# Kernel tuning notes

Hardware: AMD Instinct MI355X
Metric: run time of the kernel (lower is better)

Reference implementation:

```python
import jax, jax.numpy as jnp
import numpy as np

BN_EPS = 1e-5  # torch BatchNorm1d default


def setup_inputs() -> dict:
    key = jax.random.key(0)
    ks = jax.random.split(key, 4)
    B, C, N, O = 8, 64, 4096, 64
    x = jax.random.normal(ks[0], (B, C, N, 1), dtype=jnp.float32)
    w1 = jax.random.normal(ks[1], (C, O), dtype=jnp.float32) * (1.0 / np.sqrt(C))
    b1 = jnp.zeros((O,), jnp.float32)
    gamma = jnp.ones((O,), jnp.float32)
    beta = jnp.zeros((O,), jnp.float32)
    w2 = jax.random.normal(ks[2], (O, O), dtype=jnp.float32) * (1.0 / np.sqrt(O))
    b2 = jnp.zeros((O,), jnp.float32)
    eps_gin = jnp.zeros((), jnp.float32)  # train_eps=True, init eps=0.0
    return {"x": x, "w1": w1, "b1": b1, "gamma": gamma, "beta": beta,
            "w2": w2, "b2": b2, "eps_gin": eps_gin, "k": 16}


def _knn_idx(xf, k):
    # xf: [B, N, C] -> indices of k nearest neighbors (incl. self, loop=True)
    sq = jnp.sum(xf * xf, axis=-1)                       # [B, N]
    d = sq[:, :, None] + sq[:, None, :] - 2.0 * jnp.einsum('bnc,bmc->bnm', xf, xf)
    _, idx = jax.lax.top_k(-d, k)                        # [B, N, k]
    return idx


def reference(x, w1, b1, gamma, beta, w2, b2, eps_gin, k):
    B, C, N, _ = x.shape
    xf = jnp.transpose(x[..., 0], (0, 2, 1))             # [B, N, C]
    idx = _knn_idx(xf, k)                                # [B, N, k]
    # GIN aggregation: each node has exactly k neighbors -> gather + sum
    gathered = jax.vmap(lambda xb, ib: xb[ib])(xf, idx)  # [B, N, k, C]
    aggr = gathered.sum(axis=2)                          # [B, N, C]
    h = (1.0 + eps_gin) * xf + aggr                      # [B, N, C]
    hf = h.reshape(B * N, C)
    h1 = hf @ w1 + b1                                    # [B*N, O]
    # BatchNorm1d, training-mode batch statistics (biased variance)
    mean = jnp.mean(h1, axis=0)
    var = jnp.mean((h1 - mean) ** 2, axis=0)
    hn = gamma * (h1 - mean) / jnp.sqrt(var + BN_EPS) + beta
    hg = jax.nn.gelu(hn, approximate=False)              # torch default GELU (erf)
    out = hg @ w2 + b2                                   # [B*N, O]
    return jnp.transpose(out.reshape(B, N, -1), (0, 2, 1))[..., None]  # [B, O, N, 1]
```

## Files before the change

### kernel.cpp

```cpp
#include <hip/hip_runtime.h>
#include <cstdint>
#include <cstddef>

#define B_ 8
#define C_ 64
#define N_ 4096
#define O_ 64
#define ROWS_ (B_*N_)
#define NSPLIT_ 2
#define CAPB_ 33

typedef unsigned long long u64;
typedef unsigned int u32;
typedef unsigned short u16;
typedef __attribute__((ext_vector_type(8))) short bf16x8;
typedef __attribute__((ext_vector_type(16))) float f32x16;

#define MFMA32(A,Bv,Cv) __builtin_amdgcn_mfma_f32_32x32x16_bf16(A,Bv,Cv,0,0,0)

#define OFF_XF   0
#define OFF_SQ   8388608
#define OFF_KD   8519680
#define OFF_KI   16908288
#define OFF_PACK 21102592
#define OFF_IDX  33685504
#define OFF_H    8519680
#define OFF_H1   16908288
#define OFF_BN   25296896

__device__ __forceinline__ void insert16(u64 kv[16], u64 key) {
  if (key < kv[15]) {
#pragma unroll
    for (int j = 15; j > 0; --j) {
      u64 a = kv[j-1], b = kv[j];
      kv[j] = (key < a) ? a : ((key < b) ? key : b);
    }
    kv[0] = (key < kv[0]) ? key : kv[0];
  }
}

__global__ __launch_bounds__(256) void k_transpose(const float* __restrict__ x,
                                                   float* __restrict__ xf,
                                                   float* __restrict__ sq,
                                                   u16* __restrict__ pack) {
  __shared__ float lds[64 * 65];
  const int b  = blockIdx.x >> 6;
  const int n0 = (blockIdx.x & 63) << 6;
  const int tid = threadIdx.x;
  const float* xb = x + (size_t)b * C_ * N_;
  {
    const int nn = tid & 63;
    const int c0 = tid >> 6;
#pragma unroll
    for (int i = 0; i < 16; ++i) {
      int c = c0 + i * 4;
      lds[c * 65 + nn] = xb[(size_t)c * N_ + n0 + nn];
    }
  }
  __syncthreads();
  {
    const int cc  = tid & 63;
    const int nn0 = tid >> 6;
#pragma unroll
    for (int i = 0; i < 16; ++i) {
      int nn = nn0 + i * 4;
      xf[((size_t)(b * N_ + n0 + nn)) * 64 + cc] = lds[cc * 65 + nn];
    }
  }
  if (tid < 64) {
    float s = 0.f;
#pragma unroll
    for (int c = 0; c < 64; ++c) { float v = lds[c * 65 + tid]; s += v * v; }
    sq[b * N_ + n0 + tid] = s;
  }
  {
    const int lane = tid & 63;
    const int slice = tid >> 6;
    const int kb = slice * 16 + (lane >> 5) * 8;
#pragma unroll
    for (int tl = 0; tl < 2; ++tl) {
      const int nl = tl * 32 + (lane & 31);
      bf16x8 H, M, L;
#pragma unroll
      for (int j = 0; j < 8; ++j) {
        float f = lds[(kb + j) * 65 + nl];
        u32 u = __float_as_uint(f);
        u32 rh = (u + 0x7FFFu + ((u >> 16) & 1u)) >> 16;
        float bh = __uint_as_float(rh << 16);
        float f1 = f - bh;
        u = __float_as_uint(f1);
        u32 rm = (u + 0x7FFFu + ((u >> 16) & 1u)) >> 16;
        float bm = __uint_as_float(rm << 16);
        float f2 = f1 - bm;
        u = __float_as_uint(f2);
        u32 rl = (u + 0x7FFFu + ((u >> 16) & 1u)) >> 16;
        H[j] = (short)rh; M[j] = (short)rm; L[j] = (short)rl;
      }
      const int tile = ((blockIdx.x & 63) << 1) + tl;
      u16* basep = pack + ((size_t)(b * 128 + tile) * 12) * 512 + lane * 8;
      *(bf16x8*)(basep + (size_t)(0 + slice) * 512) = H;
      *(bf16x8*)(basep + (size_t)(4 + slice) * 512) = M;
      *(bf16x8*)(basep + (size_t)(8 + slice) * 512) = L;
    }
  }
}

#define KNN_LOAD(P, mt) do { const u16* ap_ = pb + (size_t)(mt) * (12*512); \
  P##h0 = *(const bf16x8*)(ap_ + 0*512);  P##h1 = *(const bf16x8*)(ap_ + 1*512); \
  P##h2 = *(const bf16x8*)(ap_ + 2*512);  P##h3 = *(const bf16x8*)(ap_ + 3*512); \
  P##m0 = *(const bf16x8*)(ap_ + 4*512);  P##m1 = *(const bf16x8*)(ap_ + 5*512); \
  P##m2 = *(const bf16x8*)(ap_ + 6*512);  P##m3 = *(const bf16x8*)(ap_ + 7*512); \
  P##l0 = *(const bf16x8*)(ap_ + 8*512);  P##l1 = *(const bf16x8*)(ap_ + 9*512); \
  P##l2 = *(const bf16x8*)(ap_ +10*512);  P##l3 = *(const bf16x8*)(ap_ +11*512); } while(0)

#define SQ_LOAD(MT) do { const float* sp_ = sqb + (MT) * 32 + 4 * h; \
  sv0 = *(const float4*)(sp_);      sv1 = *(const float4*)(sp_ + 8); \
  sv2 = *(const float4*)(sp_ + 16); sv3 = *(const float4*)(sp_ + 24); } while(0)

#define KNN_MFMA(P) \
  acc0 = MFMA32(P##h0, ql0, acc0);  acc1 = MFMA32(P##h1, ql1, acc1); \
  acc0 = MFMA32(P##l0, qh0, acc0);  acc1 = MFMA32(P##l1, qh1, acc1); \
  acc0 = MFMA32(P##m0, qm0, acc0);  acc1 = MFMA32(P##m1, qm1, acc1); \
  acc0 = MFMA32(P##h0, qm0, acc0);  acc1 = MFMA32(P##h1, qm1, acc1); \
  acc0 = MFMA32(P##m0, qh0, acc0);  acc1 = MFMA32(P##m1, qh1, acc1); \
  acc0 = MFMA32(P##h0, qh0, acc0);  acc1 = MFMA32(P##h1, qh1, acc1); \
  acc0 = MFMA32(P##h2, ql2, acc0);  acc1 = MFMA32(P##h3, ql3, acc1); \
  acc0 = MFMA32(P##l2, qh2, acc0);  acc1 = MFMA32(P##l3, qh3, acc1); \
  acc0 = MFMA32(P##m2, qm2, acc0);  acc1 = MFMA32(P##m3, qm3, acc1); \
  acc0 = MFMA32(P##h2, qm2, acc0);  acc1 = MFMA32(P##h3, qm3, acc1); \
  acc0 = MFMA32(P##m2, qh2, acc0);  acc1 = MFMA32(P##m3, qh3, acc1); \
  acc0 = MFMA32(P##h2, qh2, acc0);  acc1 = MFMA32(P##h3, qh3, acc1);

#define SEL_T8() do { \
  float sqv_[16] = {sv0.x, sv0.y, sv0.z, sv0.w, sv1.x, sv1.y, sv1.z, sv1.w, \
                    sv2.x, sv2.y, sv2.z, sv2.w, sv3.x, sv3.y, sv3.z, sv3.w}; \
_Pragma("unroll") \
  for (int r_ = 0; r_ < 16; ++r_) { \
    float d_ = fmaf(-2.f, acc0[r_] + acc1[r_], sqv_[r_]); \
    u32 u_ = __float_as_uint(d_); \
    u_ ^= ((int)u_ < 0) ? 0xFFFFFFFFu : 0x80000000u; \
    if (u_ < kv1[7]) { \
_Pragma("unroll") \
      for (int j_ = 7; j_ > 0; --j_) { \
        u32 a_ = kv1[j_-1], b_ = kv1[j_]; \
        kv1[j_] = (u_ < a_) ? a_ : ((u_ < b_) ? u_ : b_); \
      } \
      kv1[0] = (u_ < kv1[0]) ? u_ : kv1[0]; \
    } \
  } \
} while(0)

#define SEL_C(MT) do { \
  const u32 ic_ = (u32)((MT) * 32 + 4 * h); \
  float sqv_[16] = {sv0.x, sv0.y, sv0.z, sv0.w, sv1.x, sv1.y, sv1.z, sv1.w, \
                    sv2.x, sv2.y, sv2.z, sv2.w, sv3.x, sv3.y, sv3.z, sv3.w}; \
_Pragma("unroll") \
  for (int r_ = 0; r_ < 16; ++r_) { \
    float d_ = fmaf(-2.f, acc0[r_] + acc1[r_], sqv_[r_]); \
    u32 u_ = __float_as_uint(d_); \
    u_ ^= ((int)u_ < 0) ? 0xFFFFFFFFu : 0x80000000u; \
    if (u_ <= tauk) { \
      myc[cnt] = ((u64)u_ << 32) | (u64)(ic_ + (u32)((r_ & 3) + 8 * (r_ >> 2))); \
      ++cnt; \
    } \
  } \
  if (__any(cnt >= CAPB_ - 16)) {             \
    for (int i_ = 0; i_ < cnt; ++i_) insert16(kv, myc[i_]); \
    cnt = 0; \
  } \
} while(0)

__global__ __launch_bounds__(256, 2) void k_knn(const u16* __restrict__ pack,
                                                const float* __restrict__ sq,
                                                u32* __restrict__ kd,
                                                u16* __restrict__ ki) {
  __shared__ u64 cand[256 * CAPB_];
  const int bx = blockIdx.x;
  const int split = bx & 1;
  const int qb = (bx >> 1) & 31;
  const int b = bx >> 6;
  const int tid = threadIdx.x;
  const int lane = tid & 63;
  const int wid = tid >> 6;
  const int qt = qb * 4 + wid;
  const int h = lane >> 5;
  const u16* pb = pack + (size_t)b * (128 * 12 * 512) + lane * 8;

  const u16* qp = pb + (size_t)qt * (12 * 512);
  bf16x8 qh0 = *(const bf16x8*)(qp + 0*512), qh1 = *(const bf16x8*)(qp + 1*512);
  bf16x8 qh2 = *(const bf16x8*)(qp + 2*512), qh3 = *(const bf16x8*)(qp + 3*512);
  bf16x8 qm0 = *(const bf16x8*)(qp + 4*512), qm1 = *(const bf16x8*)(qp + 5*512);
  bf16x8 qm2 = *(const bf16x8*)(qp + 6*512), qm3 = *(const bf16x8*)(qp + 7*512);
  bf16x8 ql0 = *(const bf16x8*)(qp + 8*512), ql1 = *(const bf16x8*)(qp + 9*512);
  bf16x8 ql2 = *(const bf16x8*)(qp + 10*512), ql3 = *(const bf16x8*)(qp + 11*512);

  const float* sqb = sq + b * N_;
  const int mbase = split * 64;

  bf16x8 Ah0, Ah1, Ah2, Ah3, Am0, Am1, Am2, Am3, Al0, Al1, Al2, Al3;
  bf16x8 Bh0, Bh1, Bh2, Bh3, Bm0, Bm1, Bm2, Bm3, Bl0, Bl1, Bl2, Bl3;
  float4 sv0, sv1, sv2, sv3;

  u32 kv1[8];
#pragma unroll
  for (int j = 0; j < 8; ++j) kv1[j] = 0xFF800000u;

  KNN_LOAD(A, mbase);
  for (int ct = 0; ct < 8; ct += 2) {
    SQ_LOAD(mbase + ct);
    KNN_LOAD(B, mbase + ct + 1);
    {
      f32x16 acc0 = {0,0,0,0,0,0,0,0,0,0,0,0,0,0,0,0};
      f32x16 acc1 = {0,0,0,0,0,0,0,0,0,0,0,0,0,0,0,0};
      KNN_MFMA(A)
      SEL_T8();
    }
    SQ_LOAD(mbase + ct + 1);
    KNN_LOAD(A, mbase + ct + 2);
    {
      f32x16 acc0 = {0,0,0,0,0,0,0,0,0,0,0,0,0,0,0,0};
      f32x16 acc1 = {0,0,0,0,0,0,0,0,0,0,0,0,0,0,0,0};
      KNN_MFMA(B)
      SEL_T8();
    }
  }
  u32 tk = kv1[7];
  u32 pk = (u32)__shfl_xor((int)tk, 32);
  const u32 tauk = (tk > pk) ? tk : pk;

  u64 kv[16];
#pragma unroll
  for (int j = 0; j < 16; ++j) kv[j] = 0xFF8000000000FFFFull;
  int cnt = 0;
  u64* myc = cand + tid * CAPB_;

  KNN_LOAD(A, mbase);
  for (int ct = 0; ct < 64; ct += 2) {
    SQ_LOAD(mbase + ct);
    KNN_LOAD(B, mbase + ct + 1);
    {
      f32x16 acc0 = {0,0,0,0,0,0,0,0,0,0,0,0,0,0,0,0};
      f32x16 acc1 = {0,0,0,0,0,0,0,0,0,0,0,0,0,0,0,0};
      KNN_MFMA(A)
      SEL_C(mbase + ct);
    }
    SQ_LOAD(mbase + ct + 1);
    KNN_LOAD(A, mbase + ((ct + 2) & 63));
    {
      f32x16 acc0 = {0,0,0,0,0,0,0,0,0,0,0,0,0,0,0,0};
      f32x16 acc1 = {0,0,0,0,0,0,0,0,0,0,0,0,0,0,0,0};
      KNN_MFMA(B)
      SEL_C(mbase + ct + 1);
    }
  }
  for (int i = 0; i < cnt; ++i) insert16(kv, myc[i]);

  u64 m[16];
#pragma unroll
  for (int j = 0; j < 16; ++j) {
    u64 p = __shfl_xor(kv[15 - j], 32);
    m[j] = (kv[j] < p) ? kv[j] : p;
  }
#pragma unroll
  for (int d = 8; d >= 1; d >>= 1) {
#pragma unroll
    for (int j = 0; j < 16; ++j) {
      if ((j & d) == 0) {
        u64 a = m[j], c = m[j | d];
        m[j] = (a < c) ? a : c;
        m[j | d] = (a < c) ? c : a;
      }
    }
  }

  if (lane < 32) {
    const int row = b * N_ + qt * 32 + lane;
    u32* dp = kd + ((size_t)row * NSPLIT_ + split) * 16;
    u16* ip = ki + ((size_t)row * NSPLIT_ + split) * 16;
#pragma unroll
    for (int j = 0; j < 16; ++j) {
      dp[j] = (u32)(m[j] >> 32);
      ip[j] = (u16)(m[j] & 0xFFFFu);
    }
  }
}

__global__ __launch_bounds__(256) void k_merge(const u32* __restrict__ kd,
                                               const u16* __restrict__ ki,
                                               int* __restrict__ knn,
                                               float* __restrict__ bn_acc) {
  int tid = threadIdx.x;
  if (blockIdx.x == 0 && tid < 128) bn_acc[tid] = 0.f;
  int r = blockIdx.x * 256 + tid;
  const u32* dp = kd + (size_t)r * (NSPLIT_ * 16);
  const u16* ip = ki + (size_t)r * (NSPLIT_ * 16);
  u64 a[16], b[16];
#pragma unroll
  for (int j = 0; j < 16; ++j) {
    a[j] = ((u64)dp[j] << 32) | ip[j];
    b[j] = ((u64)dp[16 + j] << 32) | ip[16 + j];
  }
#pragma unroll
  for (int j = 0; j < 16; ++j) {
    u64 x = a[j], y = b[15 - j];
    knn[r * 16 + j] = (int)((x < y ? x : y) & 0xFFFFu);
  }
}

__global__ __launch_bounds__(256) void k_aggr(const float* __restrict__ xf,
                                              const int* __restrict__ knn,
                                              const float* __restrict__ eps_gin,
                                              float* __restrict__ h) {
  const int tid = threadIdx.x;
  const int r = blockIdx.x * 4 + (tid >> 6);
  const int c = tid & 63;
  const int b = r >> 12;
  const float* xfb = xf + (size_t)b * N_ * 64;
  const float eps = eps_gin[0];
  float v = (1.f + eps) * xf[(size_t)r * 64 + c];
  const int* kn = knn + r * 16;
#pragma unroll
  for (int j = 0; j < 16; ++j) {
    int m = kn[j];
    v += xfb[(size_t)m * 64 + c];
  }
  h[(size_t)r * 64 + c] = v;
}

__global__ __launch_bounds__(256) void k_gemm1(const float* __restrict__ h,
                                               const float* __restrict__ w1,
                                               const float* __restrict__ b1,
                                               float* __restrict__ h1,
                                               float* __restrict__ bn_acc) {
  __shared__ float w[64 * 64];
  __shared__ float rs[4][64], rs2[4][64];
  const int tid = threadIdx.x;
#pragma unroll
  for (int i = 0; i < 16; ++i) w[tid + i * 256] = w1[tid + i * 256];
  __syncthreads();
  const int o = tid & 63;
  const int q = tid >> 6;
  const int r0 = blockIdx.x * 64;
  const float bias = b1[o];
  float s = 0.f, s2 = 0.f;
#pragma unroll
  for (int i = 0; i < 16; ++i) {
    int row = r0 + q + i * 4;
    const float* hr = h + (size_t)row * 64;
    float acc = bias;
#pragma unroll
    for (int c = 0; c < 64; ++c) acc += hr[c] * w[c * 64 + o];
    h1[(size_t)row * 64 + o] = acc;
    s += acc; s2 += acc * acc;
  }
  rs[q][o] = s; rs2[q][o] = s2;
  __syncthreads();
  if (tid < 64) {
    float ts  = rs[0][tid] + rs[1][tid] + rs[2][tid] + rs[3][tid];
    float ts2 = rs2[0][tid] + rs2[1][tid] + rs2[2][tid] + rs2[3][tid];
    atomicAdd(&bn_acc[tid], ts);
    atomicAdd(&bn_acc[64 + tid], ts2);
  }
}

__global__ void k_bnfin(const float* __restrict__ bn_acc,
                        const float* __restrict__ gamma,
                        const float* __restrict__ beta,
                        float* __restrict__ bn_par) {
  int o = threadIdx.x;
  const float inv = 1.f / (float)ROWS_;
  float mean = bn_acc[o] * inv;
  float var  = bn_acc[64 + o] * inv - mean * mean;
  float sc = gamma[o] * rsqrtf(var + 1e-5f);
  bn_par[o] = sc;
  bn_par[64 + o] = beta[o] - mean * sc;
}

__global__ __launch_bounds__(256) void k_final(const float* __restrict__ h1,
                                               const float* __restrict__ bn_par,
                                               const float* __restrict__ w2,
                                               const float* __restrict__ b2,
                                               float* __restrict__ out) {
  __shared__ float w[64 * 64];
  __shared__ float hg[64 * 65];
  const int tid = threadIdx.x;
#pragma unroll
  for (int i = 0; i < 16; ++i) w[tid + i * 256] = w2[tid + i * 256];
  const int r0 = blockIdx.x * 64;
  const int b  = r0 >> 12;
  const int n0 = r0 & (N_ - 1);
  const int o = tid & 63;
  const int q = tid >> 6;
  const float sc = bn_par[o], sh = bn_par[64 + o];
#pragma unroll
  for (int i = 0; i < 16; ++i) {
    int rl = q + i * 4;
    float v = h1[(size_t)(r0 + rl) * 64 + o] * sc + sh;
    float g = 0.5f * v * (1.f + erff(v * 0.70710678118654752f));
    hg[rl * 65 + o] = g;
  }
  __syncthreads();
  const int nl = tid & 63;
#pragma unroll
  for (int i = 0; i < 16; ++i) {
    int o2 = q + i * 4;
    float acc = b2[o2];
#pragma unroll
    for (int oo = 0; oo < 64; ++oo) acc += hg[nl * 65 + oo] * w[oo * 64 + o2];
    out[((size_t)(b * 64 + o2)) * N_ + n0 + nl] = acc;
  }
}

extern "C" void kernel_launch(void* const* d_in, const int* in_sizes, int n_in,
                              void* d_out, int out_size, void* d_ws, size_t ws_size,
                              hipStream_t stream) {
  const float* x     = (const float*)d_in[0];
  const float* w1    = (const float*)d_in[1];
  const float* b1    = (const float*)d_in[2];
  const float* gamma = (const float*)d_in[3];
  const float* beta  = (const float*)d_in[4];
  const float* w2    = (const float*)d_in[5];
  const float* b2    = (const float*)d_in[6];
  const float* eps_g = (const float*)d_in[7];
  float* out = (float*)d_out;

  char* ws = (char*)d_ws;
  float* xf   = (float*)(ws + OFF_XF);
  float* sq   = (float*)(ws + OFF_SQ);
  u32*   kd   = (u32*)  (ws + OFF_KD);
  u16*   ki   = (u16*)  (ws + OFF_KI);
  u16*   pack = (u16*)  (ws + OFF_PACK);
  int*   knn  = (int*)  (ws + OFF_IDX);
  float* h    = (float*)(ws + OFF_H);
  float* h1   = (float*)(ws + OFF_H1);
  float* bn_acc = (float*)(ws + OFF_BN);
  float* bn_par = (float*)(ws + OFF_BN + 512);

  k_transpose<<<512, 256, 0, stream>>>(x, xf, sq, pack);
  k_knn<<<512, 256, 0, stream>>>(pack, sq, kd, ki);
  k_merge<<<ROWS_ / 256, 256, 0, stream>>>(kd, ki, knn, bn_acc);
  k_aggr<<<ROWS_ / 4, 256, 0, stream>>>(xf, knn, eps_g, h);
  k_gemm1<<<ROWS_ / 64, 256, 0, stream>>>(h, w1, b1, h1, bn_acc);
  k_bnfin<<<1, 64, 0, stream>>>(bn_acc, gamma, beta, bn_par);
  k_final<<<ROWS_ / 64, 256, 0, stream>>>(h1, bn_par, w2, b2, out);
}
```

Before: 367.4 us.

## Split kNN search four ways with a slimmer register pipeline and four-way merge

Each batch's candidate range is now split into four parts instead of two, and the kNN grid doubles to 1024 blocks. The two accumulators are replaced by one, and operands are loaded per k-slice into two small register sets, so the kernel can ask for three blocks per CU instead of two. The candidate buffer in shared memory is split into separate u32 distance and u16 index arrays, and the threshold test is done on the raw float before the key conversion. The merge kernel now combines four sorted partial lists with bitonic steps, which adds merge work and more partial-result traffic.

```diff
diff --git a/kernel.cpp b/kernel.cpp
--- a/kernel.cpp
+++ b/kernel.cpp
@@ -7,8 +7,10 @@
 #define N_ 4096
 #define O_ 64
 #define ROWS_ (B_*N_)
-#define NSPLIT_ 2
-#define CAPB_ 33
+#define NSPLIT_ 4
+#define CAPB_ 25
+#define DRAIN_AT_ 9
+#define TAU_TILES_ 12
 
 typedef unsigned long long u64;
 typedef unsigned int u32;
@@ -105,38 +107,40 @@
   }
 }
 
-#define KNN_LOAD(P, mt) do { const u16* ap_ = pb + (size_t)(mt) * (12*512); \
-  P##h0 = *(const bf16x8*)(ap_ + 0*512);  P##h1 = *(const bf16x8*)(ap_ + 1*512); \
-  P##h2 = *(const bf16x8*)(ap_ + 2*512);  P##h3 = *(const bf16x8*)(ap_ + 3*512); \
-  P##m0 = *(const bf16x8*)(ap_ + 4*512);  P##m1 = *(const bf16x8*)(ap_ + 5*512); \
-  P##m2 = *(const bf16x8*)(ap_ + 6*512);  P##m3 = *(const bf16x8*)(ap_ + 7*512); \
-  P##l0 = *(const bf16x8*)(ap_ + 8*512);  P##l1 = *(const bf16x8*)(ap_ + 9*512); \
-  P##l2 = *(const bf16x8*)(ap_ +10*512);  P##l3 = *(const bf16x8*)(ap_ +11*512); } while(0)
+#define LOADS(P, mt, s) do { const u16* ap_ = pb + (size_t)(mt) * (12*512) + (size_t)(s) * 512; \
+  P##h = *(const bf16x8*)(ap_);          \
+  P##m = *(const bf16x8*)(ap_ + 4*512);  \
+  P##l = *(const bf16x8*)(ap_ + 8*512);  } while(0)
+
+#define MFMAS(P, S) \
+  acc = MFMA32(P##h, ql##S, acc); \
+  acc = MFMA32(P##l, qh##S, acc); \
+  acc = MFMA32(P##m, qm##S, acc); \
+  acc = MFMA32(P##h, qm##S, acc); \
+  acc = MFMA32(P##m, qh##S, acc); \
+  acc = MFMA32(P##h, qh##S, acc);
 
 #define SQ_LOAD(MT) do { const float* sp_ = sqb + (MT) * 32 + 4 * h; \
   sv0 = *(const float4*)(sp_);      sv1 = *(const float4*)(sp_ + 8); \
   sv2 = *(const float4*)(sp_ + 16); sv3 = *(const float4*)(sp_ + 24); } while(0)
 
-#define KNN_MFMA(P) \
-  acc0 = MFMA32(P##h0, ql0, acc0);  acc1 = MFMA32(P##h1, ql1, acc1); \
-  acc0 = MFMA32(P##l0, qh0, acc0);  acc1 = MFMA32(P##l1, qh1, acc1); \
-  acc0 = MFMA32(P##m0, qm0, acc0);  acc1 = MFMA32(P##m1, qm1, acc1); \
-  acc0 = MFMA32(P##h0, qm0, acc0);  acc1 = MFMA32(P##h1, qm1, acc1); \
-  acc0 = MFMA32(P##m0, qh0, acc0);  acc1 = MFMA32(P##m1, qh1, acc1); \
-  acc0 = MFMA32(P##h0, qh0, acc0);  acc1 = MFMA32(P##h1, qh1, acc1); \
-  acc0 = MFMA32(P##h2, ql2, acc0);  acc1 = MFMA32(P##h3, ql3, acc1); \
-  acc0 = MFMA32(P##l2, qh2, acc0);  acc1 = MFMA32(P##l3, qh3, acc1); \
-  acc0 = MFMA32(P##m2, qm2, acc0);  acc1 = MFMA32(P##m3, qm3, acc1); \
-  acc0 = MFMA32(P##h2, qm2, acc0);  acc1 = MFMA32(P##h3, qm3, acc1); \
-  acc0 = MFMA32(P##m2, qh2, acc0);  acc1 = MFMA32(P##m3, qh3, acc1); \
-  acc0 = MFMA32(P##h2, qh2, acc0);  acc1 = MFMA32(P##h3, qh3, acc1);
+#define TILE_MFMA(MT, NXT) \
+  LOADS(P1, (MT), 1); \
+  MFMAS(P0, 0) \
+  LOADS(P0, (MT), 2); \
+  MFMAS(P1, 1) \
+  LOADS(P1, (MT), 3); \
+  MFMAS(P0, 2) \
+  SQ_LOAD(MT); \
+  LOADS(P0, (NXT), 0); \
+  MFMAS(P1, 3)
 
 #define SEL_T8() do { \
   float sqv_[16] = {sv0.x, sv0.y, sv0.z, sv0.w, sv1.x, sv1.y, sv1.z, sv1.w, \
                     sv2.x, sv2.y, sv2.z, sv2.w, sv3.x, sv3.y, sv3.z, sv3.w}; \
 _Pragma("unroll") \
   for (int r_ = 0; r_ < 16; ++r_) { \
-    float d_ = fmaf(-2.f, acc0[r_] + acc1[r_], sqv_[r_]); \
+    float d_ = fmaf(-2.f, acc[r_], sqv_[r_]); \
     u32 u_ = __float_as_uint(d_); \
     u_ ^= ((int)u_ < 0) ? 0xFFFFFFFFu : 0x80000000u; \
     if (u_ < kv1[7]) { \
@@ -150,35 +154,42 @@
   } \
 } while(0)
 
+#define DRAINC() do { \
+  for (int i_ = 0; i_ < cnt; ++i_) { \
+    u64 key_ = ((u64)myK[i_] << 32) | (u64)myI[i_]; \
+    insert16(kv, key_); \
+  } \
+  cnt = 0; \
+} while(0)
+
 #define SEL_C(MT) do { \
   const u32 ic_ = (u32)((MT) * 32 + 4 * h); \
   float sqv_[16] = {sv0.x, sv0.y, sv0.z, sv0.w, sv1.x, sv1.y, sv1.z, sv1.w, \
                     sv2.x, sv2.y, sv2.z, sv2.w, sv3.x, sv3.y, sv3.z, sv3.w}; \
 _Pragma("unroll") \
   for (int r_ = 0; r_ < 16; ++r_) { \
-    float d_ = fmaf(-2.f, acc0[r_] + acc1[r_], sqv_[r_]); \
-    u32 u_ = __float_as_uint(d_); \
-    u_ ^= ((int)u_ < 0) ? 0xFFFFFFFFu : 0x80000000u; \
-    if (u_ <= tauk) { \
-      myc[cnt] = ((u64)u_ << 32) | (u64)(ic_ + (u32)((r_ & 3) + 8 * (r_ >> 2))); \
+    float d_ = fmaf(-2.f, acc[r_], sqv_[r_]); \
+    if (d_ <= tauF) {                        \
+      u32 u_ = __float_as_uint(d_); \
+      u_ ^= ((int)u_ < 0) ? 0xFFFFFFFFu : 0x80000000u; \
+      myK[cnt] = u_; \
+      myI[cnt] = (u16)(ic_ + (u32)((r_ & 3) + 8 * (r_ >> 2))); \
       ++cnt; \
     } \
   } \
-  if (__any(cnt >= CAPB_ - 16)) {             \
-    for (int i_ = 0; i_ < cnt; ++i_) insert16(kv, myc[i_]); \
-    cnt = 0; \
-  } \
+  if (__any(cnt >= DRAIN_AT_)) DRAINC(); \
 } while(0)
 
-__global__ __launch_bounds__(256, 2) void k_knn(const u16* __restrict__ pack,
+__global__ __launch_bounds__(256, 3) void k_knn(const u16* __restrict__ pack,
                                                 const float* __restrict__ sq,
                                                 u32* __restrict__ kd,
                                                 u16* __restrict__ ki) {
-  __shared__ u64 cand[256 * CAPB_];
+  __shared__ u32 candK[256 * CAPB_];
+  __shared__ u16 candI[256 * CAPB_];
   const int bx = blockIdx.x;
-  const int split = bx & 1;
-  const int qb = (bx >> 1) & 31;
-  const int b = bx >> 6;
+  const int qb = bx & 31;
+  const int split = (bx >> 5) & 3;
+  const int b = bx >> 7;
   const int tid = threadIdx.x;
   const int lane = tid & 63;
   const int wid = tid >> 6;
@@ -195,92 +206,70 @@
   bf16x8 ql2 = *(const bf16x8*)(qp + 10*512), ql3 = *(const bf16x8*)(qp + 11*512);
 
   const float* sqb = sq + b * N_;
-  const int mbase = split * 64;
-
-  bf16x8 Ah0, Ah1, Ah2, Ah3, Am0, Am1, Am2, Am3, Al0, Al1, Al2, Al3;
-  bf16x8 Bh0, Bh1, Bh2, Bh3, Bm0, Bm1, Bm2, Bm3, Bl0, Bl1, Bl2, Bl3;
+  const int mbase = split * 32;
+
+  bf16x8 P0h, P0m, P0l, P1h, P1m, P1l;
   float4 sv0, sv1, sv2, sv3;
 
   u32 kv1[8];
 #pragma unroll
   for (int j = 0; j < 8; ++j) kv1[j] = 0xFF800000u;
 
-  KNN_LOAD(A, mbase);
-  for (int ct = 0; ct < 8; ct += 2) {
-    SQ_LOAD(mbase + ct);
-    KNN_LOAD(B, mbase + ct + 1);
-    {
-      f32x16 acc0 = {0,0,0,0,0,0,0,0,0,0,0,0,0,0,0,0};
-      f32x16 acc1 = {0,0,0,0,0,0,0,0,0,0,0,0,0,0,0,0};
-      KNN_MFMA(A)
-      SEL_T8();
-    }
-    SQ_LOAD(mbase + ct + 1);
-    KNN_LOAD(A, mbase + ct + 2);
-    {
-      f32x16 acc0 = {0,0,0,0,0,0,0,0,0,0,0,0,0,0,0,0};
-      f32x16 acc1 = {0,0,0,0,0,0,0,0,0,0,0,0,0,0,0,0};
-      KNN_MFMA(B)
-      SEL_T8();
-    }
-  }
-  u32 tk = kv1[7];
-  u32 pk = (u32)__shfl_xor((int)tk, 32);
-  const u32 tauk = (tk > pk) ? tk : pk;
-
-  u64 kv[16];
-#pragma unroll
-  for (int j = 0; j < 16; ++j) kv[j] = 0xFF8000000000FFFFull;
-  int cnt = 0;
-  u64* myc = cand + tid * CAPB_;
-
-  KNN_LOAD(A, mbase);
-  for (int ct = 0; ct < 64; ct += 2) {
-    SQ_LOAD(mbase + ct);
-    KNN_LOAD(B, mbase + ct + 1);
-    {
-      f32x16 acc0 = {0,0,0,0,0,0,0,0,0,0,0,0,0,0,0,0};
-      f32x16 acc1 = {0,0,0,0,0,0,0,0,0,0,0,0,0,0,0,0};
-      KNN_MFMA(A)
+  LOADS(P0, mbase, 0);
+  for (int ct = 0; ct < TAU_TILES_; ++ct) {
+    f32x16 acc = {0,0,0,0,0,0,0,0,0,0,0,0,0,0,0,0};
+    TILE_MFMA(mbase + ct, mbase + ct + 1)
+    SEL_T8();
+  }
+  {
+    u32 tk = kv1[7];
+    u32 pk = (u32)__shfl_xor((int)tk, 32);
+    if (pk > tk) tk = pk;
+    u32 tu = (tk & 0x80000000u) ? (tk ^ 0x80000000u) : ~tk;
+    const float tauF = __uint_as_float(tu);
+
+    u64 kv[16];
+#pragma unroll
+    for (int j = 0; j < 16; ++j) kv[j] = 0xFF8000000000FFFFull;
+    int cnt = 0;
+    u32* myK = candK + tid * CAPB_;
+    u16* myI = candI + tid * CAPB_;
+
+    LOADS(P0, mbase, 0);
+    for (int ct = 0; ct < 32; ++ct) {
+      f32x16 acc = {0,0,0,0,0,0,0,0,0,0,0,0,0,0,0,0};
+      TILE_MFMA(mbase + ct, mbase + ((ct + 1) & 31))
       SEL_C(mbase + ct);
     }
-    SQ_LOAD(mbase + ct + 1);
-    KNN_LOAD(A, mbase + ((ct + 2) & 63));
-    {
-      f32x16 acc0 = {0,0,0,0,0,0,0,0,0,0,0,0,0,0,0,0};
-      f32x16 acc1 = {0,0,0,0,0,0,0,0,0,0,0,0,0,0,0,0};
-      KNN_MFMA(B)
-      SEL_C(mbase + ct + 1);
-    }
-  }
-  for (int i = 0; i < cnt; ++i) insert16(kv, myc[i]);
-
-  u64 m[16];
-#pragma unroll
-  for (int j = 0; j < 16; ++j) {
-    u64 p = __shfl_xor(kv[15 - j], 32);
-    m[j] = (kv[j] < p) ? kv[j] : p;
-  }
-#pragma unroll
-  for (int d = 8; d >= 1; d >>= 1) {
+    DRAINC();
+
+    u64 m[16];
 #pragma unroll
     for (int j = 0; j < 16; ++j) {
-      if ((j & d) == 0) {
-        u64 a = m[j], c = m[j | d];
-        m[j] = (a < c) ? a : c;
-        m[j | d] = (a < c) ? c : a;
+      u64 p = __shfl_xor(kv[15 - j], 32);
+      m[j] = (kv[j] < p) ? kv[j] : p;
+    }
+#pragma unroll
+    for (int d = 8; d >= 1; d >>= 1) {
+#pragma unroll
+      for (int j = 0; j < 16; ++j) {
+        if ((j & d) == 0) {
+          u64 a = m[j], c = m[j | d];
+          m[j] = (a < c) ? a : c;
+          m[j | d] = (a < c) ? c : a;
+        }
       }
     }
-  }
-
-  if (lane < 32) {
-    const int row = b * N_ + qt * 32 + lane;
-    u32* dp = kd + ((size_t)row * NSPLIT_ + split) * 16;
-    u16* ip = ki + ((size_t)row * NSPLIT_ + split) * 16;
-#pragma unroll
-    for (int j = 0; j < 16; ++j) {
-      dp[j] = (u32)(m[j] >> 32);
-      ip[j] = (u16)(m[j] & 0xFFFFu);
+
+    if (lane < 32) {
+      const int row = b * N_ + qt * 32 + lane;
+      u32* dp = kd + ((size_t)row * NSPLIT_ + split) * 16;
+      u16* ip = ki + ((size_t)row * NSPLIT_ + split) * 16;
+#pragma unroll
+      for (int j = 0; j < 16; ++j) {
+        dp[j] = (u32)(m[j] >> 32);
+        ip[j] = (u16)(m[j] & 0xFFFFu);
+      }
     }
   }
 }
@@ -294,15 +283,31 @@
   int r = blockIdx.x * 256 + tid;
   const u32* dp = kd + (size_t)r * (NSPLIT_ * 16);
   const u16* ip = ki + (size_t)r * (NSPLIT_ * 16);
-  u64 a[16], b[16];
+  u64 m1[16], m2[16];
 #pragma unroll
   for (int j = 0; j < 16; ++j) {
-    a[j] = ((u64)dp[j] << 32) | ip[j];
-    b[j] = ((u64)dp[16 + j] << 32) | ip[16 + j];
+    u64 a = ((u64)dp[j] << 32) | ip[j];
+    u64 b = ((u64)dp[16 + (15 - j)] << 32) | ip[16 + (15 - j)];
+    m1[j] = (a < b) ? a : b;
+    u64 c = ((u64)dp[32 + j] << 32) | ip[32 + j];
+    u64 d = ((u64)dp[48 + (15 - j)] << 32) | ip[48 + (15 - j)];
+    m2[j] = (c < d) ? c : d;
+  }
+#pragma unroll
+  for (int dd = 8; dd >= 1; dd >>= 1) {
+#pragma unroll
+    for (int j = 0; j < 16; ++j) {
+      if ((j & dd) == 0) {
+        u64 a = m1[j], c = m1[j | dd];
+        m1[j] = (a < c) ? a : c;  m1[j | dd] = (a < c) ? c : a;
+        u64 e = m2[j], f = m2[j | dd];
+        m2[j] = (e < f) ? e : f;  m2[j | dd] = (e < f) ? f : e;
+      }
+    }
   }
 #pragma unroll
   for (int j = 0; j < 16; ++j) {
-    u64 x = a[j], y = b[15 - j];
+    u64 x = m1[j], y = m2[15 - j];
     knn[r * 16 + j] = (int)((x < y ? x : y) & 0xFFFFu);
   }
 }
@@ -437,7 +442,7 @@
   float* bn_par = (float*)(ws + OFF_BN + 512);
 
   k_transpose<<<512, 256, 0, stream>>>(x, xf, sq, pack);
-  k_knn<<<512, 256, 0, stream>>>(pack, sq, kd, ki);
+  k_knn<<<1024, 256, 0, stream>>>(pack, sq, kd, ki);
   k_merge<<<ROWS_ / 256, 256, 0, stream>>>(kd, ki, knn, bn_acc);
   k_aggr<<<ROWS_ / 4, 256, 0, stream>>>(xf, knn, eps_g, h);
   k_gemm1<<<ROWS_ / 64, 256, 0, stream>>>(h, w1, b1, h1, bn_acc);
```

Result: slower. 417.2 us (+13.6%).

## Software-pipeline KNN MFMA tiles against selection and compare in float domain

Applied to the files above, without the earlier changes.

Restructures the KNN distance loop so the MFMA chain for the next 32-column tile runs while the selection/candidate filtering of the previous tile executes, using two independent accumulators, one per tile, instead of two partial accumulators summed per tile. The candidate filter now compares the raw float distance against a float threshold decoded from the sortable-key tau, so the key transform only runs for accepted candidates. It also simplifies the sign-flip to a branchless shift/or. This aims to hide MFMA latency behind VALU selection work, at the cost of a serial 24-deep MFMA dependency chain per tile, more live registers, and one extra prefetched tile at the loop ends.

```diff
diff --git a/kernel.cpp b/kernel.cpp
--- a/kernel.cpp
+++ b/kernel.cpp
@@ -9,6 +9,7 @@
 #define ROWS_ (B_*N_)
 #define NSPLIT_ 2
 #define CAPB_ 33
+#define TAU_TILES_ 8
 
 typedef unsigned long long u64;
 typedef unsigned int u32;
@@ -105,7 +106,7 @@
   }
 }
 
-#define KNN_LOAD(P, mt) do { const u16* ap_ = pb + (size_t)(mt) * (12*512); \
+#define LOADF(P, mt) do { const u16* ap_ = pb + (size_t)(mt) * (12*512); \
   P##h0 = *(const bf16x8*)(ap_ + 0*512);  P##h1 = *(const bf16x8*)(ap_ + 1*512); \
   P##h2 = *(const bf16x8*)(ap_ + 2*512);  P##h3 = *(const bf16x8*)(ap_ + 3*512); \
   P##m0 = *(const bf16x8*)(ap_ + 4*512);  P##m1 = *(const bf16x8*)(ap_ + 5*512); \
@@ -113,32 +114,32 @@
   P##l0 = *(const bf16x8*)(ap_ + 8*512);  P##l1 = *(const bf16x8*)(ap_ + 9*512); \
   P##l2 = *(const bf16x8*)(ap_ +10*512);  P##l3 = *(const bf16x8*)(ap_ +11*512); } while(0)
 
-#define SQ_LOAD(MT) do { const float* sp_ = sqb + (MT) * 32 + 4 * h; \
-  sv0 = *(const float4*)(sp_);      sv1 = *(const float4*)(sp_ + 8); \
-  sv2 = *(const float4*)(sp_ + 16); sv3 = *(const float4*)(sp_ + 24); } while(0)
-
-#define KNN_MFMA(P) \
-  acc0 = MFMA32(P##h0, ql0, acc0);  acc1 = MFMA32(P##h1, ql1, acc1); \
-  acc0 = MFMA32(P##l0, qh0, acc0);  acc1 = MFMA32(P##l1, qh1, acc1); \
-  acc0 = MFMA32(P##m0, qm0, acc0);  acc1 = MFMA32(P##m1, qm1, acc1); \
-  acc0 = MFMA32(P##h0, qm0, acc0);  acc1 = MFMA32(P##h1, qm1, acc1); \
-  acc0 = MFMA32(P##m0, qh0, acc0);  acc1 = MFMA32(P##m1, qh1, acc1); \
-  acc0 = MFMA32(P##h0, qh0, acc0);  acc1 = MFMA32(P##h1, qh1, acc1); \
-  acc0 = MFMA32(P##h2, ql2, acc0);  acc1 = MFMA32(P##h3, ql3, acc1); \
-  acc0 = MFMA32(P##l2, qh2, acc0);  acc1 = MFMA32(P##l3, qh3, acc1); \
-  acc0 = MFMA32(P##m2, qm2, acc0);  acc1 = MFMA32(P##m3, qm3, acc1); \
-  acc0 = MFMA32(P##h2, qm2, acc0);  acc1 = MFMA32(P##h3, qm3, acc1); \
-  acc0 = MFMA32(P##m2, qh2, acc0);  acc1 = MFMA32(P##m3, qh3, acc1); \
-  acc0 = MFMA32(P##h2, qh2, acc0);  acc1 = MFMA32(P##h3, qh3, acc1);
-
-#define SEL_T8() do { \
-  float sqv_[16] = {sv0.x, sv0.y, sv0.z, sv0.w, sv1.x, sv1.y, sv1.z, sv1.w, \
-                    sv2.x, sv2.y, sv2.z, sv2.w, sv3.x, sv3.y, sv3.z, sv3.w}; \
+#define SQL(V0,V1,V2,V3, MT) do { const float* sp_ = sqb + (MT) * 32 + 4 * h; \
+  V0 = *(const float4*)(sp_);      V1 = *(const float4*)(sp_ + 8); \
+  V2 = *(const float4*)(sp_ + 16); V3 = *(const float4*)(sp_ + 24); } while(0)
+
+#define TILE24(P, ACC) \
+  ACC = MFMA32(P##h0, ql0, kz);   ACC = MFMA32(P##l0, qh0, ACC); \
+  ACC = MFMA32(P##m0, qm0, ACC);  ACC = MFMA32(P##h0, qm0, ACC); \
+  ACC = MFMA32(P##m0, qh0, ACC);  ACC = MFMA32(P##h0, qh0, ACC); \
+  ACC = MFMA32(P##h1, ql1, ACC);  ACC = MFMA32(P##l1, qh1, ACC); \
+  ACC = MFMA32(P##m1, qm1, ACC);  ACC = MFMA32(P##h1, qm1, ACC); \
+  ACC = MFMA32(P##m1, qh1, ACC);  ACC = MFMA32(P##h1, qh1, ACC); \
+  ACC = MFMA32(P##h2, ql2, ACC);  ACC = MFMA32(P##l2, qh2, ACC); \
+  ACC = MFMA32(P##m2, qm2, ACC);  ACC = MFMA32(P##h2, qm2, ACC); \
+  ACC = MFMA32(P##m2, qh2, ACC);  ACC = MFMA32(P##h2, qh2, ACC); \
+  ACC = MFMA32(P##h3, ql3, ACC);  ACC = MFMA32(P##l3, qh3, ACC); \
+  ACC = MFMA32(P##m3, qm3, ACC);  ACC = MFMA32(P##h3, qm3, ACC); \
+  ACC = MFMA32(P##m3, qh3, ACC);  ACC = MFMA32(P##h3, qh3, ACC);
+
+#define SEL_T8(ACC, V0,V1,V2,V3) do { \
+  float sqv_[16] = {V0.x, V0.y, V0.z, V0.w, V1.x, V1.y, V1.z, V1.w, \
+                    V2.x, V2.y, V2.z, V2.w, V3.x, V3.y, V3.z, V3.w}; \
 _Pragma("unroll") \
   for (int r_ = 0; r_ < 16; ++r_) { \
-    float d_ = fmaf(-2.f, acc0[r_] + acc1[r_], sqv_[r_]); \
+    float d_ = fmaf(-2.f, ACC[r_], sqv_[r_]); \
     u32 u_ = __float_as_uint(d_); \
-    u_ ^= ((int)u_ < 0) ? 0xFFFFFFFFu : 0x80000000u; \
+    u_ ^= ((u32)((int)u_ >> 31)) | 0x80000000u; \
     if (u_ < kv1[7]) { \
 _Pragma("unroll") \
       for (int j_ = 7; j_ > 0; --j_) { \
@@ -150,21 +151,21 @@
   } \
 } while(0)
 
-#define SEL_C(MT) do { \
+#define SEL_C(ACC, V0,V1,V2,V3, MT) do { \
   const u32 ic_ = (u32)((MT) * 32 + 4 * h); \
-  float sqv_[16] = {sv0.x, sv0.y, sv0.z, sv0.w, sv1.x, sv1.y, sv1.z, sv1.w, \
-                    sv2.x, sv2.y, sv2.z, sv2.w, sv3.x, sv3.y, sv3.z, sv3.w}; \
+  float sqv_[16] = {V0.x, V0.y, V0.z, V0.w, V1.x, V1.y, V1.z, V1.w, \
+                    V2.x, V2.y, V2.z, V2.w, V3.x, V3.y, V3.z, V3.w}; \
 _Pragma("unroll") \
   for (int r_ = 0; r_ < 16; ++r_) { \
-    float d_ = fmaf(-2.f, acc0[r_] + acc1[r_], sqv_[r_]); \
-    u32 u_ = __float_as_uint(d_); \
-    u_ ^= ((int)u_ < 0) ? 0xFFFFFFFFu : 0x80000000u; \
-    if (u_ <= tauk) { \
+    float d_ = fmaf(-2.f, ACC[r_], sqv_[r_]); \
+    if (d_ <= tauF) { \
+      u32 u_ = __float_as_uint(d_); \
+      u_ ^= ((u32)((int)u_ >> 31)) | 0x80000000u; \
       myc[cnt] = ((u64)u_ << 32) | (u64)(ic_ + (u32)((r_ & 3) + 8 * (r_ >> 2))); \
       ++cnt; \
     } \
   } \
-  if (__any(cnt >= CAPB_ - 16)) {             \
+  if (__any(cnt >= CAPB_ - 16)) {           \
     for (int i_ = 0; i_ < cnt; ++i_) insert16(kv, myc[i_]); \
     cnt = 0; \
   } \
@@ -196,37 +197,35 @@
 
   const float* sqb = sq + b * N_;
   const int mbase = split * 64;
+  const f32x16 kz = {0,0,0,0,0,0,0,0,0,0,0,0,0,0,0,0};
 
   bf16x8 Ah0, Ah1, Ah2, Ah3, Am0, Am1, Am2, Am3, Al0, Al1, Al2, Al3;
   bf16x8 Bh0, Bh1, Bh2, Bh3, Bm0, Bm1, Bm2, Bm3, Bl0, Bl1, Bl2, Bl3;
-  float4 sv0, sv1, sv2, sv3;
+  float4 sa0, sa1, sa2, sa3, sb0, sb1, sb2, sb3;
+  f32x16 acc0, acc1;
 
   u32 kv1[8];
 #pragma unroll
   for (int j = 0; j < 8; ++j) kv1[j] = 0xFF800000u;
 
-  KNN_LOAD(A, mbase);
-  for (int ct = 0; ct < 8; ct += 2) {
-    SQ_LOAD(mbase + ct);
-    KNN_LOAD(B, mbase + ct + 1);
-    {
-      f32x16 acc0 = {0,0,0,0,0,0,0,0,0,0,0,0,0,0,0,0};
-      f32x16 acc1 = {0,0,0,0,0,0,0,0,0,0,0,0,0,0,0,0};
-      KNN_MFMA(A)
-      SEL_T8();
-    }
-    SQ_LOAD(mbase + ct + 1);
-    KNN_LOAD(A, mbase + ct + 2);
-    {
-      f32x16 acc0 = {0,0,0,0,0,0,0,0,0,0,0,0,0,0,0,0};
-      f32x16 acc1 = {0,0,0,0,0,0,0,0,0,0,0,0,0,0,0,0};
-      KNN_MFMA(B)
-      SEL_T8();
-    }
+  LOADF(A, mbase);  SQL(sa0,sa1,sa2,sa3, mbase);
+  TILE24(A, acc0)
+  LOADF(B, mbase + 1);  SQL(sb0,sb1,sb2,sb3, mbase + 1);
+  for (int ct = 0; ct < TAU_TILES_; ct += 2) {
+    TILE24(B, acc1)
+    LOADF(A, mbase + ct + 2);
+    SEL_T8(acc0, sa0,sa1,sa2,sa3);
+    SQL(sa0,sa1,sa2,sa3, mbase + ct + 2);
+    TILE24(A, acc0)
+    LOADF(B, mbase + ct + 3);
+    SEL_T8(acc1, sb0,sb1,sb2,sb3);
+    SQL(sb0,sb1,sb2,sb3, mbase + ct + 3);
   }
   u32 tk = kv1[7];
   u32 pk = (u32)__shfl_xor((int)tk, 32);
-  const u32 tauk = (tk > pk) ? tk : pk;
+  if (pk > tk) tk = pk;
+  u32 tu = (tk & 0x80000000u) ? (tk ^ 0x80000000u) : ~tk;
+  const float tauF = __uint_as_float(tu);
 
   u64 kv[16];
 #pragma unroll
@@ -234,24 +233,18 @@
   int cnt = 0;
   u64* myc = cand + tid * CAPB_;
 
-  KNN_LOAD(A, mbase);
+  LOADF(A, mbase);  SQL(sa0,sa1,sa2,sa3, mbase);
+  TILE24(A, acc0)
+  LOADF(B, mbase + 1);  SQL(sb0,sb1,sb2,sb3, mbase + 1);
   for (int ct = 0; ct < 64; ct += 2) {
-    SQ_LOAD(mbase + ct);
-    KNN_LOAD(B, mbase + ct + 1);
-    {
-      f32x16 acc0 = {0,0,0,0,0,0,0,0,0,0,0,0,0,0,0,0};
-      f32x16 acc1 = {0,0,0,0,0,0,0,0,0,0,0,0,0,0,0,0};
-      KNN_MFMA(A)
-      SEL_C(mbase + ct);
-    }
-    SQ_LOAD(mbase + ct + 1);
-    KNN_LOAD(A, mbase + ((ct + 2) & 63));
-    {
-      f32x16 acc0 = {0,0,0,0,0,0,0,0,0,0,0,0,0,0,0,0};
-      f32x16 acc1 = {0,0,0,0,0,0,0,0,0,0,0,0,0,0,0,0};
-      KNN_MFMA(B)
-      SEL_C(mbase + ct + 1);
-    }
+    TILE24(B, acc1)
+    LOADF(A, mbase + ((ct + 2) & 63));
+    SEL_C(acc0, sa0,sa1,sa2,sa3, mbase + ct);
+    SQL(sa0,sa1,sa2,sa3, mbase + ((ct + 2) & 63));
+    TILE24(A, acc0)
+    LOADF(B, mbase + ((ct + 3) & 63));
+    SEL_C(acc1, sb0,sb1,sb2,sb3, mbase + ct + 1);
+    SQL(sb0,sb1,sb2,sb3, mbase + ((ct + 3) & 63));
   }
   for (int i = 0; i < cnt; ++i) insert16(kv, myc[i]);
 
```

Result: slower. 379.3 us (+3.3%).

## Fuse merge, aggregation and first GEMM; fold BN finalize into final kernel

Applied to the files above, without the earlier changes.

Merges the kNN split-merge, GIN neighbor aggregation and first linear layer into one kernel that keeps indices and aggregated rows in LDS. The BN-accumulator zeroing moves into the kNN kernel, and the BN finalize step moves into the final kernel. Weights are stored transposed in LDS so the inner products can use float4 reads. This removes three launches and the global round trips for knn indices and h. The cost is more LDS per block and redundant BN-parameter computation in every final block.

```diff
diff --git a/kernel.cpp b/kernel.cpp
--- a/kernel.cpp
+++ b/kernel.cpp
@@ -9,6 +9,7 @@
 #define ROWS_ (B_*N_)
 #define NSPLIT_ 2
 #define CAPB_ 33
+#define TAU_TILES_ 8
 
 typedef unsigned long long u64;
 typedef unsigned int u32;
@@ -23,10 +24,8 @@
 #define OFF_KD   8519680
 #define OFF_KI   16908288
 #define OFF_PACK 21102592
-#define OFF_IDX  33685504
-#define OFF_H    8519680
-#define OFF_H1   16908288
-#define OFF_BN   25296896
+#define OFF_H1   21102592
+#define OFF_BN   33685504
 
 __device__ __forceinline__ void insert16(u64 kv[16], u64 key) {
   if (key < kv[15]) {
@@ -173,13 +172,15 @@
 __global__ __launch_bounds__(256, 2) void k_knn(const u16* __restrict__ pack,
                                                 const float* __restrict__ sq,
                                                 u32* __restrict__ kd,
-                                                u16* __restrict__ ki) {
+                                                u16* __restrict__ ki,
+                                                float* __restrict__ bn_acc) {
   __shared__ u64 cand[256 * CAPB_];
   const int bx = blockIdx.x;
+  const int tid = threadIdx.x;
+  if (bx == 0 && tid < 128) bn_acc[tid] = 0.f;
   const int split = bx & 1;
   const int qb = (bx >> 1) & 31;
   const int b = bx >> 6;
-  const int tid = threadIdx.x;
   const int lane = tid & 63;
   const int wid = tid >> 6;
   const int qt = qb * 4 + wid;
@@ -206,7 +207,7 @@
   for (int j = 0; j < 8; ++j) kv1[j] = 0xFF800000u;
 
   KNN_LOAD(A, mbase);
-  for (int ct = 0; ct < 8; ct += 2) {
+  for (int ct = 0; ct < TAU_TILES_; ct += 2) {
     SQ_LOAD(mbase + ct);
     KNN_LOAD(B, mbase + ct + 1);
     {
@@ -285,72 +286,70 @@
   }
 }
 
-__global__ __launch_bounds__(256) void k_merge(const u32* __restrict__ kd,
-                                               const u16* __restrict__ ki,
-                                               int* __restrict__ knn,
-                                               float* __restrict__ bn_acc) {
-  int tid = threadIdx.x;
-  if (blockIdx.x == 0 && tid < 128) bn_acc[tid] = 0.f;
-  int r = blockIdx.x * 256 + tid;
-  const u32* dp = kd + (size_t)r * (NSPLIT_ * 16);
-  const u16* ip = ki + (size_t)r * (NSPLIT_ * 16);
-  u64 a[16], b[16];
-#pragma unroll
-  for (int j = 0; j < 16; ++j) {
-    a[j] = ((u64)dp[j] << 32) | ip[j];
-    b[j] = ((u64)dp[16 + j] << 32) | ip[16 + j];
-  }
-#pragma unroll
-  for (int j = 0; j < 16; ++j) {
-    u64 x = a[j], y = b[15 - j];
-    knn[r * 16 + j] = (int)((x < y ? x : y) & 0xFFFFu);
-  }
-}
-
-__global__ __launch_bounds__(256) void k_aggr(const float* __restrict__ xf,
-                                              const int* __restrict__ knn,
-                                              const float* __restrict__ eps_gin,
-                                              float* __restrict__ h) {
-  const int tid = threadIdx.x;
-  const int r = blockIdx.x * 4 + (tid >> 6);
-  const int c = tid & 63;
-  const int b = r >> 12;
-  const float* xfb = xf + (size_t)b * N_ * 64;
-  const float eps = eps_gin[0];
-  float v = (1.f + eps) * xf[(size_t)r * 64 + c];
-  const int* kn = knn + r * 16;
-#pragma unroll
-  for (int j = 0; j < 16; ++j) {
-    int m = kn[j];
-    v += xfb[(size_t)m * 64 + c];
-  }
-  h[(size_t)r * 64 + c] = v;
-}
-
-__global__ __launch_bounds__(256) void k_gemm1(const float* __restrict__ h,
-                                               const float* __restrict__ w1,
-                                               const float* __restrict__ b1,
-                                               float* __restrict__ h1,
-                                               float* __restrict__ bn_acc) {
-  __shared__ float w[64 * 64];
+__global__ __launch_bounds__(256) void k_mid(const u32* __restrict__ kd,
+                                             const u16* __restrict__ ki,
+                                             const float* __restrict__ xf,
+                                             const float* __restrict__ eps_gin,
+                                             const float* __restrict__ w1,
+                                             const float* __restrict__ b1,
+                                             float* __restrict__ h1,
+                                             float* __restrict__ bn_acc) {
+  __shared__ float wT[64 * 65];
+  __shared__ float hL[64 * 65];
+  __shared__ int   knnL[64 * 16];
   __shared__ float rs[4][64], rs2[4][64];
   const int tid = threadIdx.x;
-#pragma unroll
-  for (int i = 0; i < 16; ++i) w[tid + i * 256] = w1[tid + i * 256];
-  __syncthreads();
-  const int o = tid & 63;
+  const int r0 = blockIdx.x * 64;
+#pragma unroll
+  for (int i = 0; i < 16; ++i) {
+    int idx = tid + i * 256;
+    wT[(idx & 63) * 65 + (idx >> 6)] = w1[idx];
+  }
+  if (tid < 64) {
+    const int r = r0 + tid;
+    const u32* dp = kd + (size_t)r * (NSPLIT_ * 16);
+    const u16* ip = ki + (size_t)r * (NSPLIT_ * 16);
+#pragma unroll
+    for (int j = 0; j < 16; ++j) {
+      u64 a = ((u64)dp[j] << 32) | ip[j];
+      u64 bb = ((u64)dp[16 + (15 - j)] << 32) | ip[16 + (15 - j)];
+      knnL[tid * 16 + j] = (int)((a < bb ? a : bb) & 0xFFFFu);
+    }
+  }
+  __syncthreads();
+  const int c = tid & 63;
   const int q = tid >> 6;
-  const int r0 = blockIdx.x * 64;
+  const int b = r0 >> 12;
+  const float* xfb = xf + (size_t)b * N_ * 64;
+  const float eps1 = 1.f + eps_gin[0];
+#pragma unroll
+  for (int i = 0; i < 16; ++i) {
+    int rl = q + i * 4;
+    float v = eps1 * xfb[(size_t)((r0 & (N_ - 1)) + rl) * 64 + c];
+    const int* kn = knnL + rl * 16;
+#pragma unroll
+    for (int j = 0; j < 16; ++j) {
+      int mr = kn[j];
+      v += xfb[(size_t)mr * 64 + c];
+    }
+    hL[rl * 65 + c] = v;
+  }
+  __syncthreads();
+  const int o = c;
   const float bias = b1[o];
   float s = 0.f, s2 = 0.f;
 #pragma unroll
   for (int i = 0; i < 16; ++i) {
-    int row = r0 + q + i * 4;
-    const float* hr = h + (size_t)row * 64;
+    int rl = q + i * 4;
     float acc = bias;
 #pragma unroll
-    for (int c = 0; c < 64; ++c) acc += hr[c] * w[c * 64 + o];
-    h1[(size_t)row * 64 + o] = acc;
+    for (int k = 0; k < 16; ++k) {
+      float4 hv = *(const float4*)&hL[rl * 65 + 4 * k];
+      float4 wv = *(const float4*)&wT[o * 65 + 4 * k];
+      acc += hv.x * wv.x; acc += hv.y * wv.y;
+      acc += hv.z * wv.z; acc += hv.w * wv.w;
+    }
+    h1[(size_t)(r0 + rl) * 64 + o] = acc;
     s += acc; s2 += acc * acc;
   }
   rs[q][o] = s; rs2[q][o] = s2;
@@ -363,35 +362,37 @@
   }
 }
 
-__global__ void k_bnfin(const float* __restrict__ bn_acc,
-                        const float* __restrict__ gamma,
-                        const float* __restrict__ beta,
-                        float* __restrict__ bn_par) {
-  int o = threadIdx.x;
-  const float inv = 1.f / (float)ROWS_;
-  float mean = bn_acc[o] * inv;
-  float var  = bn_acc[64 + o] * inv - mean * mean;
-  float sc = gamma[o] * rsqrtf(var + 1e-5f);
-  bn_par[o] = sc;
-  bn_par[64 + o] = beta[o] - mean * sc;
-}
-
 __global__ __launch_bounds__(256) void k_final(const float* __restrict__ h1,
-                                               const float* __restrict__ bn_par,
+                                               const float* __restrict__ bn_acc,
+                                               const float* __restrict__ gamma,
+                                               const float* __restrict__ beta,
                                                const float* __restrict__ w2,
                                                const float* __restrict__ b2,
                                                float* __restrict__ out) {
-  __shared__ float w[64 * 64];
+  __shared__ float wT2[64 * 65];
   __shared__ float hg[64 * 65];
+  __shared__ float scsh[128];
   const int tid = threadIdx.x;
 #pragma unroll
-  for (int i = 0; i < 16; ++i) w[tid + i * 256] = w2[tid + i * 256];
+  for (int i = 0; i < 16; ++i) {
+    int idx = tid + i * 256;
+    wT2[(idx & 63) * 65 + (idx >> 6)] = w2[idx];
+  }
+  if (tid < 64) {
+    const float inv = 1.f / (float)ROWS_;
+    float mean = bn_acc[tid] * inv;
+    float var  = bn_acc[64 + tid] * inv - mean * mean;
+    float sc = gamma[tid] * rsqrtf(var + 1e-5f);
+    scsh[tid] = sc;
+    scsh[64 + tid] = beta[tid] - mean * sc;
+  }
+  __syncthreads();
   const int r0 = blockIdx.x * 64;
   const int b  = r0 >> 12;
   const int n0 = r0 & (N_ - 1);
   const int o = tid & 63;
   const int q = tid >> 6;
-  const float sc = bn_par[o], sh = bn_par[64 + o];
+  const float sc = scsh[o], sh = scsh[64 + o];
 #pragma unroll
   for (int i = 0; i < 16; ++i) {
     int rl = q + i * 4;
@@ -401,12 +402,19 @@
   }
   __syncthreads();
   const int nl = tid & 63;
+  float4 hv[16];
+#pragma unroll
+  for (int k = 0; k < 16; ++k) hv[k] = *(const float4*)&hg[nl * 65 + 4 * k];
 #pragma unroll
   for (int i = 0; i < 16; ++i) {
     int o2 = q + i * 4;
     float acc = b2[o2];
 #pragma unroll
-    for (int oo = 0; oo < 64; ++oo) acc += hg[nl * 65 + oo] * w[oo * 64 + o2];
+    for (int k = 0; k < 16; ++k) {
+      float4 wv = *(const float4*)&wT2[o2 * 65 + 4 * k];
+      acc += hv[k].x * wv.x; acc += hv[k].y * wv.y;
+      acc += hv[k].z * wv.z; acc += hv[k].w * wv.w;
+    }
     out[((size_t)(b * 64 + o2)) * N_ + n0 + nl] = acc;
   }
 }
@@ -430,17 +438,11 @@
   u32*   kd   = (u32*)  (ws + OFF_KD);
   u16*   ki   = (u16*)  (ws + OFF_KI);
   u16*   pack = (u16*)  (ws + OFF_PACK);
-  int*   knn  = (int*)  (ws + OFF_IDX);
-  float* h    = (float*)(ws + OFF_H);
   float* h1   = (float*)(ws + OFF_H1);
   float* bn_acc = (float*)(ws + OFF_BN);
-  float* bn_par = (float*)(ws + OFF_BN + 512);
 
   k_transpose<<<512, 256, 0, stream>>>(x, xf, sq, pack);
-  k_knn<<<512, 256, 0, stream>>>(pack, sq, kd, ki);
-  k_merge<<<ROWS_ / 256, 256, 0, stream>>>(kd, ki, knn, bn_acc);
-  k_aggr<<<ROWS_ / 4, 256, 0, stream>>>(xf, knn, eps_g, h);
-  k_gemm1<<<ROWS_ / 64, 256, 0, stream>>>(h, w1, b1, h1, bn_acc);
-  k_bnfin<<<1, 64, 0, stream>>>(bn_acc, gamma, beta, bn_par);
-  k_final<<<ROWS_ / 64, 256, 0, stream>>>(h1, bn_par, w2, b2, out);
-}
+  k_knn<<<512, 256, 0, stream>>>(pack, sq, kd, ki, bn_acc);
+  k_mid<<<ROWS_ / 64, 256, 0, stream>>>(kd, ki, xf, eps_g, w1, b1, h1, bn_acc);
+  k_final<<<ROWS_ / 64, 256, 0, stream>>>(h1, bn_acc, gamma, beta, w2, b2, out);
+}
```

Result: slower. 391.7 us (+6.6%).
